# Kernel optimization log

Measured on AMD Instinct MI355X. Metric: run time of the kernel, lower is better.

## Reference

```python
import jax, jax.numpy as jnp
import numpy as np

EPS_COS = 1e-8   # torch F.cosine_similarity eps
EPS_L1 = 1e-12   # torch F.normalize eps


def setup_inputs() -> dict:
    key = jax.random.key(0)
    k1, k2, k3, k4 = jax.random.split(key, 4)
    B, D, C = 32768, 768, 200
    features = jax.random.normal(k1, (B, D), dtype=jnp.float32)
    centers = jax.random.normal(k2, (C, D), dtype=jnp.float32)
    labels = jax.random.randint(k3, (B,), 0, C)
    labelled_or_not = jax.random.randint(k4, (B,), 0, 2).astype(jnp.bool_)
    return {"features": features, "centers": centers, "labels": labels,
            "labelled_or_not": labelled_or_not}


def reference(features, centers, labels, labelled_or_not):
    # cosine similarity: x.y / (max(|x|,eps) * max(|y|,eps))
    fn = features / jnp.maximum(jnp.linalg.norm(features, axis=1, keepdims=True), EPS_COS)
    cn = centers / jnp.maximum(jnp.linalg.norm(centers, axis=1, keepdims=True), EPS_COS)
    cos = jnp.einsum('bd,cd->bc', fn, cn)  # [B, C]

    # per-sample sign logic: label column -> +|cos|, all others -> -|cos|
    a = jnp.abs(cos)
    is_label = jax.nn.one_hot(labels, cos.shape[1], dtype=jnp.bool_)  # [B, C]
    signed = jnp.where(is_label, a, -a)

    # L1 normalize per row (||row||_1 == sum of |cos| regardless of signs)
    l1 = jnp.sum(a, axis=1, keepdims=True)
    normed = signed / jnp.maximum(l1, EPS_L1)

    # only labelled rows contribute (row-wise normalize is independent per row,
    # so masking after is equivalent to boolean-indexing before)
    contrib = jnp.where(labelled_or_not[:, None], normed, 0.0)
    return -jnp.sum(contrib)
```

## Files before the change

kernel.cpp:

```cpp
#include <hip/hip_runtime.h>
#include <hip/hip_bf16.h>

#define NROWS 32768
#define DIMS  768
#define NC    200
#define CPAD  256
#define KSTEP 32
#define NSTEP (DIMS / KSTEP)
#define ROWSB 64

typedef __attribute__((ext_vector_type(8))) short short8;
typedef __attribute__((ext_vector_type(4))) float f32x4;

__device__ __forceinline__ unsigned pk_bf16(float lo, float hi) {
  union { __hip_bfloat162 h; unsigned u; } c;
  c.h = __float22bfloat162_rn(make_float2(lo, hi));
  return c.u;
}

__device__ __forceinline__ void glds16(const void* g, void* l) {
  __builtin_amdgcn_global_load_lds(
      (const __attribute__((address_space(1))) unsigned int*)g,
      (__attribute__((address_space(3))) unsigned int*)l, 16, 0, 0);
}

__global__ __launch_bounds__(256) void prep_centers_k(const float* __restrict__ centers,
                                                      short* __restrict__ cnb2,
                                                      float* __restrict__ out) {
  const int c = blockIdx.x;
  const int tid = threadIdx.x;
  if (c == 0 && tid == 0) out[0] = 0.f;
  const int cswz = (c >> 1) & 3;
  if (c >= NC) {
    for (int d = tid; d < DIMS; d += 256)
      cnb2[(d >> 5) * (CPAD * KSTEP) + c * KSTEP + d % 32] = 0;
    return;
  }
  float ssq = 0.f;
  for (int d = tid; d < DIMS; d += 256) {
    float v = centers[c * DIMS + d];
    ssq += v * v;
  }
#pragma unroll
  for (int off = 32; off > 0; off >>= 1) ssq += __shfl_down(ssq, off);
  __shared__ float red[4];
  const int wid = tid >> 6, lane = tid & 63;
  if (lane == 0) red[wid] = ssq;
  __syncthreads();
  const float tot = red[0] + red[1] + red[2] + red[3];
  const float inv = 1.f / fmaxf(sqrtf(tot), 1e-8f);
  for (int d = tid; d < DIMS; d += 256) {
    const float v = centers[c * DIMS + d] * inv;
    union { __hip_bfloat16 h; short s; } cv;
    cv.h = __float2bfloat16(v);
    const int ks = d >> 5, dk = d & 31, q = dk >> 3, j = dk & 7;
    cnb2[ks * (CPAD * KSTEP) + c * KSTEP + ((q ^ cswz) * 8 + j)] = cv.s;
  }
}

__global__ __launch_bounds__(256) void cos_loss_k(
    const float* __restrict__ feats,
    const short* __restrict__ cnb2,
    const int* __restrict__ labels,
    const int* __restrict__ labelled,
    float* __restrict__ out) {
  const int tid = threadIdx.x;
  const int w = tid >> 6;
  const int lane = tid & 63;
  const int m = lane & 15;
  const int kg = lane >> 4;
  const int sq = (kg ^ ((m >> 1) & 3)) * 8;
  const int rowBase = blockIdx.x * ROWSB;

  __shared__ short As[2][ROWSB][32];
  __shared__ short Bs[2][CPAD][32];
  __shared__ float invs[ROWSB];
  __shared__ int   labLds[ROWSB];
  __shared__ int   lblLds[ROWSB];
  __shared__ float l1part[4][ROWSB];
  __shared__ float alpart[4][ROWSB];

  if (tid < ROWSB) {
    labLds[tid] = labels[rowBase + tid];
    lblLds[tid] = labelled[rowBase + tid];
  }

  const int arow = tid >> 2;
  const int aq   = tid & 3;
  const int aswz = (arow >> 1) & 3;
  const float* asrc = feats + (size_t)(rowBase + arow) * DIMS + aq * 8;
  short* adst[2] = { &As[0][arow][(aq ^ aswz) * 8], &As[1][arow][(aq ^ aswz) * 8] };
  const short* bbase = cnb2 + (size_t)(w * 64) * KSTEP + lane * 8;

  f32x4 acc[4][4];
#pragma unroll
  for (int mi = 0; mi < 4; ++mi)
#pragma unroll
    for (int ni = 0; ni < 4; ++ni) acc[mi][ni] = (f32x4){0.f, 0.f, 0.f, 0.f};

  float ssq = 0.f;
  float4 S0_lo, S0_hi, S1_lo, S1_hi;

#define LOADA(P, step) do {                                              \
    const float* ap_ = asrc + (step) * KSTEP;                            \
    P##_lo = *(const float4*)(ap_);                                      \
    P##_hi = *(const float4*)(ap_ + 4);                                  \
  } while (0)

#define WRITEA(P, buf) do {                                              \
    ssq += P##_lo.x*P##_lo.x + P##_lo.y*P##_lo.y                         \
         + P##_lo.z*P##_lo.z + P##_lo.w*P##_lo.w;                        \
    ssq += P##_hi.x*P##_hi.x + P##_hi.y*P##_hi.y                         \
         + P##_hi.z*P##_hi.z + P##_hi.w*P##_hi.w;                        \
    union { short8 s; unsigned u[4]; } p_;                               \
    p_.u[0] = pk_bf16(P##_lo.x, P##_lo.y);                               \
    p_.u[1] = pk_bf16(P##_lo.z, P##_lo.w);                               \
    p_.u[2] = pk_bf16(P##_hi.x, P##_hi.y);                               \
    p_.u[3] = pk_bf16(P##_hi.z, P##_hi.w);                               \
    *(short8*)(adst[(buf)]) = p_.s;                                      \
  } while (0)

#define DMAB(step, buf) do {                                             \
    const short* g_ = bbase + (size_t)(step) * (CPAD * KSTEP);           \
    glds16(g_ + 0 * (16 * KSTEP), &Bs[(buf)][w * 64 + 0 * 16][0]);       \
    glds16(g_ + 1 * (16 * KSTEP), &Bs[(buf)][w * 64 + 1 * 16][0]);       \
    glds16(g_ + 2 * (16 * KSTEP), &Bs[(buf)][w * 64 + 2 * 16][0]);       \
    glds16(g_ + 3 * (16 * KSTEP), &Bs[(buf)][w * 64 + 3 * 16][0]);       \
  } while (0)

#define COMPUTE(buf) do {                                                \
    short8 af[4], bf[4];                                                 \
    _Pragma("unroll")                                                    \
    for (int mi = 0; mi < 4; ++mi)                                       \
      af[mi] = *(const short8*)(&As[(buf)][mi * 16 + m][sq]);            \
    _Pragma("unroll")                                                    \
    for (int ni = 0; ni < 4; ++ni)                                       \
      bf[ni] = *(const short8*)(&Bs[(buf)][w * 64 + ni * 16 + m][sq]);   \
    _Pragma("unroll")                                                    \
    for (int mi = 0; mi < 4; ++mi)                                       \
      _Pragma("unroll")                                                  \
      for (int ni = 0; ni < 4; ++ni)                                     \
        acc[mi][ni] = __builtin_amdgcn_mfma_f32_16x16x32_bf16(           \
            af[mi], bf[ni], acc[mi][ni], 0, 0, 0);                       \
  } while (0)

  LOADA(S0, 0);
  LOADA(S1, 1);
  DMAB(0, 0);
  WRITEA(S0, 0);
  __syncthreads();

  for (int ks = 0; ks < NSTEP; ks += 2) {
    DMAB(ks + 1, 1);
    if (ks + 2 < NSTEP) LOADA(S0, ks + 2);
    WRITEA(S1, 1);
    COMPUTE(0);
    __syncthreads();
    if (ks + 2 < NSTEP) {
      DMAB(ks + 2, 0);
      if (ks + 3 < NSTEP) LOADA(S1, ks + 3);
      WRITEA(S0, 0);
    }
    COMPUTE(1);
    __syncthreads();
  }

#undef LOADA
#undef WRITEA
#undef DMAB
#undef COMPUTE

  ssq += __shfl_xor(ssq, 1);
  ssq += __shfl_xor(ssq, 2);
  if ((tid & 3) == 0) invs[arow] = 1.f / fmaxf(sqrtf(ssq), 1e-8f);
  __syncthreads();

#pragma unroll
  for (int mi = 0; mi < 4; ++mi) {
    float l1r[4] = {0.f, 0.f, 0.f, 0.f};
    float alr[4] = {0.f, 0.f, 0.f, 0.f};
    float iv[4];
    int labr[4];
#pragma unroll
    for (int r = 0; r < 4; ++r) {
      const int row = mi * 16 + kg * 4 + r;
      iv[r] = invs[row];
      labr[r] = labLds[row];
    }
#pragma unroll
    for (int ni = 0; ni < 4; ++ni) {
      const int col = w * 64 + ni * 16 + m;
#pragma unroll
      for (int r = 0; r < 4; ++r) {
        const float a = fabsf(acc[mi][ni][r] * iv[r]);
        l1r[r] += a;
        if (col == labr[r]) alr[r] += a;
      }
    }
#pragma unroll
    for (int r = 0; r < 4; ++r) {
#pragma unroll
      for (int off = 1; off < 16; off <<= 1) {
        l1r[r] += __shfl_xor(l1r[r], off);
        alr[r] += __shfl_xor(alr[r], off);
      }
    }
    if (m == 0) {
#pragma unroll
      for (int r = 0; r < 4; ++r) {
        l1part[w][mi * 16 + kg * 4 + r] = l1r[r];
        alpart[w][mi * 16 + kg * 4 + r] = alr[r];
      }
    }
  }
  __syncthreads();

  if (tid < ROWSB) {
    const float L = l1part[0][tid] + l1part[1][tid] + l1part[2][tid] + l1part[3][tid];
    const float A = alpart[0][tid] + alpart[1][tid] + alpart[2][tid] + alpart[3][tid];
    float c = lblLds[tid] ? (L - 2.f * A) / fmaxf(L, 1e-12f) : 0.f;
#pragma unroll
    for (int off = 1; off < 64; off <<= 1) c += __shfl_xor(c, off);
    if (tid == 0) atomicAdd(out, c);
  }
}

extern "C" void kernel_launch(void* const* d_in, const int* in_sizes, int n_in,
                              void* d_out, int out_size, void* d_ws, size_t ws_size,
                              hipStream_t stream) {
  const float* feats = (const float*)d_in[0];
  const float* centers = (const float*)d_in[1];
  const int* labels = (const int*)d_in[2];
  const int* labelled = (const int*)d_in[3];
  float* out = (float*)d_out;
  short* cnb2 = (short*)d_ws;

  prep_centers_k<<<CPAD, 256, 0, stream>>>(centers, cnb2, out);
  cos_loss_k<<<NROWS / ROWSB, 256, 0, stream>>>(feats, cnb2, labels, labelled, out);
}
```

Measured before the change: 38.41 us.

## Replace full syncthreads with explicit vmcnt waits and raw barriers in GEMM pipeline

Restructures the main loop into uniform phases that issue the next B DMA and the A prefetch two steps ahead, compute the current buffer, then wait on precise vmcnt counts before writing A to LDS and hitting a raw s_barrier. Out-of-range steps are clamped to the last step instead of branched around, and the sum-of-squares is guarded so it is not double counted. The aim is to keep global loads in flight across the barrier rather than having __syncthreads drain every outstanding memory op, and to make the loop body branch-free. The cost is some redundant loads at the tail and correctness that depends on hand-counted waitcnt values and compiler ordering.

```diff
diff --git a/kernel.cpp b/kernel.cpp
--- a/kernel.cpp
+++ b/kernel.cpp
@@ -11,6 +11,11 @@
 
 typedef __attribute__((ext_vector_type(8))) short short8;
 typedef __attribute__((ext_vector_type(4))) float f32x4;
+
+#define SFENCE    asm volatile("" ::: "memory")
+#define WAITV2    asm volatile("s_waitcnt vmcnt(2)" ::: "memory")
+#define WAITV6    asm volatile("s_waitcnt vmcnt(6)" ::: "memory")
+#define WAITV2L0  asm volatile("s_waitcnt vmcnt(2) lgkmcnt(0)" ::: "memory")
 
 __device__ __forceinline__ unsigned pk_bf16(float lo, float hi) {
   union { __hip_bfloat162 h; unsigned u; } c;
@@ -107,11 +112,13 @@
     P##_hi = *(const float4*)(ap_ + 4);                                  \
   } while (0)
 
-#define WRITEA(P, buf) do {                                              \
-    ssq += P##_lo.x*P##_lo.x + P##_lo.y*P##_lo.y                         \
-         + P##_lo.z*P##_lo.z + P##_lo.w*P##_lo.w;                        \
-    ssq += P##_hi.x*P##_hi.x + P##_hi.y*P##_hi.y                         \
-         + P##_hi.z*P##_hi.z + P##_hi.w*P##_hi.w;                        \
+#define WRITEA(P, buf, guard) do {                                       \
+    if (guard) {                                                         \
+      ssq += P##_lo.x*P##_lo.x + P##_lo.y*P##_lo.y                       \
+           + P##_lo.z*P##_lo.z + P##_lo.w*P##_lo.w;                      \
+      ssq += P##_hi.x*P##_hi.x + P##_hi.y*P##_hi.y                       \
+           + P##_hi.z*P##_hi.z + P##_hi.w*P##_hi.w;                      \
+    }                                                                    \
     union { short8 s; unsigned u[4]; } p_;                               \
     p_.u[0] = pk_bf16(P##_lo.x, P##_lo.y);                               \
     p_.u[1] = pk_bf16(P##_lo.z, P##_lo.w);                               \
@@ -144,31 +151,40 @@
             af[mi], bf[ni], acc[mi][ni], 0, 0, 0);                       \
   } while (0)
 
+#define PHASE(s, CUR, NXT, SCONS, SLOAD) do {                            \
+    const int sn_ = ((s) + 1 < NSTEP) ? (s) + 1 : NSTEP - 1;             \
+    const int sl_ = ((s) + 2 < NSTEP) ? (s) + 2 : NSTEP - 1;             \
+    DMAB(sn_, NXT);                                                      \
+    SFENCE;                                                              \
+    LOADA(SLOAD, sl_);                                                   \
+    SFENCE;                                                              \
+    COMPUTE(CUR);                                                        \
+    WAITV6;                                                              \
+    WRITEA(SCONS, NXT, (s) + 1 < NSTEP);                                 \
+    WAITV2L0;                                                            \
+    __builtin_amdgcn_s_barrier();                                        \
+  } while (0)
+
+  DMAB(0, 0);
+  SFENCE;
   LOADA(S0, 0);
   LOADA(S1, 1);
-  DMAB(0, 0);
-  WRITEA(S0, 0);
-  __syncthreads();
+  SFENCE;
+  WAITV2;
+  WRITEA(S0, 0, true);
+  WAITV2L0;
+  __builtin_amdgcn_s_barrier();
 
   for (int ks = 0; ks < NSTEP; ks += 2) {
-    DMAB(ks + 1, 1);
-    if (ks + 2 < NSTEP) LOADA(S0, ks + 2);
-    WRITEA(S1, 1);
-    COMPUTE(0);
-    __syncthreads();
-    if (ks + 2 < NSTEP) {
-      DMAB(ks + 2, 0);
-      if (ks + 3 < NSTEP) LOADA(S1, ks + 3);
-      WRITEA(S0, 0);
-    }
-    COMPUTE(1);
-    __syncthreads();
+    PHASE(ks,     0, 1, S1, S0);
+    PHASE(ks + 1, 1, 0, S0, S1);
   }
 
 #undef LOADA
 #undef WRITEA
 #undef DMAB
 #undef COMPUTE
+#undef PHASE
 
   ssq += __shfl_xor(ssq, 1);
   ssq += __shfl_xor(ssq, 2);
```

After: 39.12 us. No clear change (+1.8%).

## Warp-specialize cos kernel into producer and MFMA consumer waves

Applied to the files above, without the earlier changes.

Each block grows to 512 threads. Four producer waves load fp32 features, accumulate squared norms and write bf16 tiles to LDS. Four consumer waves stream the pre-normalized center tiles straight from global memory into registers instead of staging them through LDS, and run the MFMAs. The two groups synchronise through raw s_barrier and hand-placed waitcnt instructions, and the swizzle on the center layout is dropped. The aim is to overlap the global feature loads and bf16 conversion with matrix math and to cut LDS traffic for B. The price is fragile manual synchronisation and more redundant global and L2 reads of the centers.

```diff
diff --git a/kernel.cpp b/kernel.cpp
--- a/kernel.cpp
+++ b/kernel.cpp
@@ -12,16 +12,15 @@
 typedef __attribute__((ext_vector_type(8))) short short8;
 typedef __attribute__((ext_vector_type(4))) float f32x4;
 
+#define WAITV4 asm volatile("s_waitcnt vmcnt(4)" ::: "memory")
+#define WAITV2 asm volatile("s_waitcnt vmcnt(2)" ::: "memory")
+#define WAITL0 asm volatile("s_waitcnt lgkmcnt(0)" ::: "memory")
+#define BAR    __builtin_amdgcn_s_barrier()
+
 __device__ __forceinline__ unsigned pk_bf16(float lo, float hi) {
   union { __hip_bfloat162 h; unsigned u; } c;
   c.h = __float22bfloat162_rn(make_float2(lo, hi));
   return c.u;
-}
-
-__device__ __forceinline__ void glds16(const void* g, void* l) {
-  __builtin_amdgcn_global_load_lds(
-      (const __attribute__((address_space(1))) unsigned int*)g,
-      (__attribute__((address_space(3))) unsigned int*)l, 16, 0, 0);
 }
 
 __global__ __launch_bounds__(256) void prep_centers_k(const float* __restrict__ centers,
@@ -30,10 +29,9 @@
   const int c = blockIdx.x;
   const int tid = threadIdx.x;
   if (c == 0 && tid == 0) out[0] = 0.f;
-  const int cswz = (c >> 1) & 3;
   if (c >= NC) {
     for (int d = tid; d < DIMS; d += 256)
-      cnb2[(d >> 5) * (CPAD * KSTEP) + c * KSTEP + d % 32] = 0;
+      cnb2[(d >> 5) * (CPAD * KSTEP) + c * KSTEP + (d & 31)] = 0;
     return;
   }
   float ssq = 0.f;
@@ -53,27 +51,22 @@
     const float v = centers[c * DIMS + d] * inv;
     union { __hip_bfloat16 h; short s; } cv;
     cv.h = __float2bfloat16(v);
-    const int ks = d >> 5, dk = d & 31, q = dk >> 3, j = dk & 7;
-    cnb2[ks * (CPAD * KSTEP) + c * KSTEP + ((q ^ cswz) * 8 + j)] = cv.s;
-  }
-}
-
-__global__ __launch_bounds__(256) void cos_loss_k(
+    cnb2[(d >> 5) * (CPAD * KSTEP) + c * KSTEP + (d & 31)] = cv.s;
+  }
+}
+
+__global__ __launch_bounds__(512, 4) void cos_loss_k(
     const float* __restrict__ feats,
     const short* __restrict__ cnb2,
     const int* __restrict__ labels,
     const int* __restrict__ labelled,
     float* __restrict__ out) {
   const int tid = threadIdx.x;
-  const int w = tid >> 6;
+  const int wid = tid >> 6;
   const int lane = tid & 63;
-  const int m = lane & 15;
-  const int kg = lane >> 4;
-  const int sq = (kg ^ ((m >> 1) & 3)) * 8;
   const int rowBase = blockIdx.x * ROWSB;
 
   __shared__ short As[2][ROWSB][32];
-  __shared__ short Bs[2][CPAD][32];
   __shared__ float invs[ROWSB];
   __shared__ int   labLds[ROWSB];
   __shared__ int   lblLds[ROWSB];
@@ -85,134 +78,161 @@
     lblLds[tid] = labelled[rowBase + tid];
   }
 
-  const int arow = tid >> 2;
-  const int aq   = tid & 3;
-  const int aswz = (arow >> 1) & 3;
-  const float* asrc = feats + (size_t)(rowBase + arow) * DIMS + aq * 8;
-  short* adst[2] = { &As[0][arow][(aq ^ aswz) * 8], &As[1][arow][(aq ^ aswz) * 8] };
-  const short* bbase = cnb2 + (size_t)(w * 64) * KSTEP + lane * 8;
-
-  f32x4 acc[4][4];
-#pragma unroll
-  for (int mi = 0; mi < 4; ++mi)
-#pragma unroll
-    for (int ni = 0; ni < 4; ++ni) acc[mi][ni] = (f32x4){0.f, 0.f, 0.f, 0.f};
-
-  float ssq = 0.f;
-  float4 S0_lo, S0_hi, S1_lo, S1_hi;
-
-#define LOADA(P, step) do {                                              \
-    const float* ap_ = asrc + (step) * KSTEP;                            \
-    P##_lo = *(const float4*)(ap_);                                      \
-    P##_hi = *(const float4*)(ap_ + 4);                                  \
-  } while (0)
-
-#define WRITEA(P, buf) do {                                              \
-    ssq += P##_lo.x*P##_lo.x + P##_lo.y*P##_lo.y                         \
-         + P##_lo.z*P##_lo.z + P##_lo.w*P##_lo.w;                        \
-    ssq += P##_hi.x*P##_hi.x + P##_hi.y*P##_hi.y                         \
-         + P##_hi.z*P##_hi.z + P##_hi.w*P##_hi.w;                        \
-    union { short8 s; unsigned u[4]; } p_;                               \
-    p_.u[0] = pk_bf16(P##_lo.x, P##_lo.y);                               \
-    p_.u[1] = pk_bf16(P##_lo.z, P##_lo.w);                               \
-    p_.u[2] = pk_bf16(P##_hi.x, P##_hi.y);                               \
-    p_.u[3] = pk_bf16(P##_hi.z, P##_hi.w);                               \
-    *(short8*)(adst[(buf)]) = p_.s;                                      \
-  } while (0)
-
-#define DMAB(step, buf) do {                                             \
-    const short* g_ = bbase + (size_t)(step) * (CPAD * KSTEP);           \
-    glds16(g_ + 0 * (16 * KSTEP), &Bs[(buf)][w * 64 + 0 * 16][0]);       \
-    glds16(g_ + 1 * (16 * KSTEP), &Bs[(buf)][w * 64 + 1 * 16][0]);       \
-    glds16(g_ + 2 * (16 * KSTEP), &Bs[(buf)][w * 64 + 2 * 16][0]);       \
-    glds16(g_ + 3 * (16 * KSTEP), &Bs[(buf)][w * 64 + 3 * 16][0]);       \
-  } while (0)
-
-#define COMPUTE(buf) do {                                                \
-    short8 af[4], bf[4];                                                 \
+  if (wid < 4) {
+    const int m = lane & 15;
+    const int kg = lane >> 4;
+    const int rdq = (kg ^ ((m >> 1) & 3)) * 8;
+    const short* bp = cnb2 + (size_t)(wid * 64 + m) * KSTEP + kg * 8;
+
+    f32x4 acc[4][4];
+#pragma unroll
+    for (int mi = 0; mi < 4; ++mi)
+#pragma unroll
+      for (int ni = 0; ni < 4; ++ni) acc[mi][ni] = (f32x4){0.f, 0.f, 0.f, 0.f};
+
+    short8 B0[4], B1[4];
+
+#define LOADB(B, s) do {                                                 \
+    const short* bs_ = bp + (size_t)(s) * (CPAD * KSTEP);                \
+    B[0] = *(const short8*)(bs_ + 0 * (16 * KSTEP));                     \
+    B[1] = *(const short8*)(bs_ + 1 * (16 * KSTEP));                     \
+    B[2] = *(const short8*)(bs_ + 2 * (16 * KSTEP));                     \
+    B[3] = *(const short8*)(bs_ + 3 * (16 * KSTEP));                     \
+  } while (0)
+
+#define CCOMPUTE(ab, B) do {                                             \
+    short8 af[4];                                                        \
     _Pragma("unroll")                                                    \
     for (int mi = 0; mi < 4; ++mi)                                       \
-      af[mi] = *(const short8*)(&As[(buf)][mi * 16 + m][sq]);            \
-    _Pragma("unroll")                                                    \
-    for (int ni = 0; ni < 4; ++ni)                                       \
-      bf[ni] = *(const short8*)(&Bs[(buf)][w * 64 + ni * 16 + m][sq]);   \
+      af[mi] = *(const short8*)(&As[(ab)][mi * 16 + m][rdq]);            \
     _Pragma("unroll")                                                    \
     for (int mi = 0; mi < 4; ++mi)                                       \
       _Pragma("unroll")                                                  \
       for (int ni = 0; ni < 4; ++ni)                                     \
         acc[mi][ni] = __builtin_amdgcn_mfma_f32_16x16x32_bf16(           \
-            af[mi], bf[ni], acc[mi][ni], 0, 0, 0);                       \
-  } while (0)
-
-  LOADA(S0, 0);
-  LOADA(S1, 1);
-  DMAB(0, 0);
-  WRITEA(S0, 0);
-  __syncthreads();
-
-  for (int ks = 0; ks < NSTEP; ks += 2) {
-    DMAB(ks + 1, 1);
-    if (ks + 2 < NSTEP) LOADA(S0, ks + 2);
-    WRITEA(S1, 1);
-    COMPUTE(0);
-    __syncthreads();
-    if (ks + 2 < NSTEP) {
-      DMAB(ks + 2, 0);
-      if (ks + 3 < NSTEP) LOADA(S1, ks + 3);
-      WRITEA(S0, 0);
+            af[mi], B[ni], acc[mi][ni], 0, 0, 0);                        \
+  } while (0)
+
+    LOADB(B0, 0);
+    LOADB(B1, 1);
+    WAITV4;
+    BAR;
+
+    for (int s = 0; s < NSTEP; s += 2) {
+      CCOMPUTE(0, B0);
+      { const int s2 = (s + 2 < NSTEP) ? s + 2 : NSTEP - 1; LOADB(B0, s2); }
+      WAITV4;
+      BAR;
+      CCOMPUTE(1, B1);
+      { const int s3 = (s + 3 < NSTEP) ? s + 3 : NSTEP - 1; LOADB(B1, s3); }
+      WAITV4;
+      BAR;
     }
-    COMPUTE(1);
-    __syncthreads();
-  }
-
+#undef LOADB
+#undef CCOMPUTE
+
+    BAR;
+
+#pragma unroll
+    for (int mi = 0; mi < 4; ++mi) {
+      float l1r[4] = {0.f, 0.f, 0.f, 0.f};
+      float alr[4] = {0.f, 0.f, 0.f, 0.f};
+      float iv[4];
+      int labr[4];
+#pragma unroll
+      for (int r = 0; r < 4; ++r) {
+        const int row = mi * 16 + kg * 4 + r;
+        iv[r] = invs[row];
+        labr[r] = labLds[row];
+      }
+#pragma unroll
+      for (int ni = 0; ni < 4; ++ni) {
+        const int col = wid * 64 + ni * 16 + m;
+#pragma unroll
+        for (int r = 0; r < 4; ++r) {
+          const float a = fabsf(acc[mi][ni][r] * iv[r]);
+          l1r[r] += a;
+          if (col == labr[r]) alr[r] += a;
+        }
+      }
+#pragma unroll
+      for (int r = 0; r < 4; ++r) {
+#pragma unroll
+        for (int off = 1; off < 16; off <<= 1) {
+          l1r[r] += __shfl_xor(l1r[r], off);
+          alr[r] += __shfl_xor(alr[r], off);
+        }
+      }
+      if (m == 0) {
+#pragma unroll
+        for (int r = 0; r < 4; ++r) {
+          l1part[wid][mi * 16 + kg * 4 + r] = l1r[r];
+          alpart[wid][mi * 16 + kg * 4 + r] = alr[r];
+        }
+      }
+    }
+  } else {
+    const int pt = (wid - 4) * 64 + lane;
+    const int arow = pt >> 2;
+    const int aq   = pt & 3;
+    const int aswz = (arow >> 1) & 3;
+    const float* asrc = feats + (size_t)(rowBase + arow) * DIMS + aq * 8;
+    short* adst0 = &As[0][arow][(aq ^ aswz) * 8];
+    short* adst1 = &As[1][arow][(aq ^ aswz) * 8];
+
+    float ssq = 0.f;
+    float4 S0lo, S0hi, S1lo, S1hi;
+
+#define LOADA(P, s) do {                                                 \
+    const float* ap_ = asrc + (s) * KSTEP;                               \
+    P##lo = *(const float4*)(ap_);                                       \
+    P##hi = *(const float4*)(ap_ + 4);                                   \
+  } while (0)
+
+#define WRITEA(P, dst, guard) do {                                       \
+    if (guard) {                                                         \
+      ssq += P##lo.x*P##lo.x + P##lo.y*P##lo.y                           \
+           + P##lo.z*P##lo.z + P##lo.w*P##lo.w;                          \
+      ssq += P##hi.x*P##hi.x + P##hi.y*P##hi.y                           \
+           + P##hi.z*P##hi.z + P##hi.w*P##hi.w;                          \
+    }                                                                    \
+    union { short8 s8; unsigned u[4]; } p_;                              \
+    p_.u[0] = pk_bf16(P##lo.x, P##lo.y);                                 \
+    p_.u[1] = pk_bf16(P##lo.z, P##lo.w);                                 \
+    p_.u[2] = pk_bf16(P##hi.x, P##hi.y);                                 \
+    p_.u[3] = pk_bf16(P##hi.z, P##hi.w);                                 \
+    *(short8*)(dst) = p_.s8;                                             \
+  } while (0)
+
+    LOADA(S0, 0);
+    LOADA(S1, 1);
+    WAITV2;
+    WRITEA(S0, adst0, true);
+    WAITL0;
+    BAR;
+
+    for (int s = 0; s < NSTEP; s += 2) {
+      { const int s2 = (s + 2 < NSTEP) ? s + 2 : NSTEP - 1; LOADA(S0, s2); }
+      WAITV2;
+      WRITEA(S1, adst1, (s + 1 < NSTEP));
+      WAITL0;
+      BAR;
+      { const int s3 = (s + 3 < NSTEP) ? s + 3 : NSTEP - 1; LOADA(S1, s3); }
+      WAITV2;
+      WRITEA(S0, adst0, (s + 2 < NSTEP));
+      WAITL0;
+      BAR;
+    }
 #undef LOADA
 #undef WRITEA
-#undef DMAB
-#undef COMPUTE
-
-  ssq += __shfl_xor(ssq, 1);
-  ssq += __shfl_xor(ssq, 2);
-  if ((tid & 3) == 0) invs[arow] = 1.f / fmaxf(sqrtf(ssq), 1e-8f);
-  __syncthreads();
-
-#pragma unroll
-  for (int mi = 0; mi < 4; ++mi) {
-    float l1r[4] = {0.f, 0.f, 0.f, 0.f};
-    float alr[4] = {0.f, 0.f, 0.f, 0.f};
-    float iv[4];
-    int labr[4];
-#pragma unroll
-    for (int r = 0; r < 4; ++r) {
-      const int row = mi * 16 + kg * 4 + r;
-      iv[r] = invs[row];
-      labr[r] = labLds[row];
-    }
-#pragma unroll
-    for (int ni = 0; ni < 4; ++ni) {
-      const int col = w * 64 + ni * 16 + m;
-#pragma unroll
-      for (int r = 0; r < 4; ++r) {
-        const float a = fabsf(acc[mi][ni][r] * iv[r]);
-        l1r[r] += a;
-        if (col == labr[r]) alr[r] += a;
-      }
-    }
-#pragma unroll
-    for (int r = 0; r < 4; ++r) {
-#pragma unroll
-      for (int off = 1; off < 16; off <<= 1) {
-        l1r[r] += __shfl_xor(l1r[r], off);
-        alr[r] += __shfl_xor(alr[r], off);
-      }
-    }
-    if (m == 0) {
-#pragma unroll
-      for (int r = 0; r < 4; ++r) {
-        l1part[w][mi * 16 + kg * 4 + r] = l1r[r];
-        alpart[w][mi * 16 + kg * 4 + r] = alr[r];
-      }
-    }
-  }
+
+    ssq += __shfl_xor(ssq, 1);
+    ssq += __shfl_xor(ssq, 2);
+    if ((lane & 3) == 0) invs[arow] = 1.f / fmaxf(sqrtf(ssq), 1e-8f);
+    WAITL0;
+    BAR;
+  }
+
   __syncthreads();
 
   if (tid < ROWSB) {
@@ -236,5 +256,5 @@
   short* cnb2 = (short*)d_ws;
 
   prep_centers_k<<<CPAD, 256, 0, stream>>>(centers, cnb2, out);
-  cos_loss_k<<<NROWS / ROWSB, 256, 0, stream>>>(feats, cnb2, labels, labelled, out);
-}
+  cos_loss_k<<<NROWS / ROWSB, 512, 0, stream>>>(feats, cnb2, labels, labelled, out);
+}
```

Result: faster. 35.90 us (-6.5%).
